# Kernel tuning notes

Hardware: AMD Instinct MI355X
Metric: run time of the kernel (lower is better)

The kernel has to match this reference:

```python
import jax, jax.numpy as jnp
import numpy as np

EPS = 1e-6

def rms_norm(x, w):
    xf = x.astype(jnp.float32)
    xf = xf * jax.lax.rsqrt(jnp.mean(jnp.square(xf), axis=-1, keepdims=True) + EPS)
    return xf.astype(x.dtype) * w

def rotate_pairs(x):
    x = x.reshape(*x.shape[:-1], -1, 2)
    x1, x2 = x[..., 0], x[..., 1]
    return jnp.stack((-x2, x1), axis=-1).reshape(*x.shape[:-2], -1)

def apply_rope_axis(x, coords, inv_freq):
    # x: [B, H, T, axis_width]; coords: [T]; inv_freq: [axis_dim]
    angles = coords[:, None].astype(jnp.float32) * inv_freq[None, :]  # [T, axis_dim]
    cos = jnp.repeat(jnp.cos(angles), 2, axis=-1).astype(x.dtype)  # [T, axis_width]
    sin = jnp.repeat(jnp.sin(angles), 2, axis=-1).astype(x.dtype)
    return x * cos[None, None] + rotate_pairs(x) * sin[None, None]

def modulate(x, shift, scale):
    return x * (1.0 + scale[:, None, :]) + shift[:, None, :]

def setup_inputs() -> dict:
    key = jax.random.key(0)
    ks = jax.random.split(key, 16)
    B, T, D = 2, 2048, 1024
    HD = 64            # head_dim
    HID = 4096         # swiglu hidden (dim * mlp_ratio)
    CD = 1024          # cond_dim
    s = lambda n: 1.0 / np.sqrt(n)
    return {
        "x": jax.random.normal(ks[0], (B, T, D), jnp.float32),
        "cond": jax.random.normal(ks[1], (B, CD), jnp.float32),
        "norm1_w": jnp.ones((D,), jnp.float32),
        "qkv_w": jax.random.normal(ks[2], (3 * D, D), jnp.float32) * s(D),
        "q_norm_w": jnp.ones((HD,), jnp.float32),
        "k_norm_w": jnp.ones((HD,), jnp.float32),
        "proj_w": jax.random.normal(ks[3], (D, D), jnp.float32) * s(D),
        "proj_b": jnp.zeros((D,), jnp.float32),
        "norm2_w": jnp.ones((D,), jnp.float32),
        "fc1_w": jax.random.normal(ks[4], (2 * HID, D), jnp.float32) * s(D),
        "fc1_b": jnp.zeros((2 * HID,), jnp.float32),
        "fc2_w": jax.random.normal(ks[5], (D, HID), jnp.float32) * s(HID),
        "fc2_b": jnp.zeros((D,), jnp.float32),
        "ada_w": jax.random.normal(ks[6], (6 * D, CD), jnp.float32) * 0.02,
        "ada_b": jnp.zeros((6 * D,), jnp.float32),
        "height": 64,
        "width": 32,
    }

def reference(x, cond, norm1_w, qkv_w, q_norm_w, k_norm_w, proj_w, proj_b,
              norm2_w, fc1_w, fc1_b, fc2_w, fc2_b, ada_w, ada_b, height, width):
    B, T, D = x.shape
    HD = q_norm_w.shape[0]
    NH = D // HD
    scale = HD ** -0.5
    axis_dim = HD // 4
    axis_w = axis_dim * 2
    inv_freq = 1.0 / (10000.0 ** (jnp.arange(axis_dim, dtype=jnp.float32) / axis_dim))

    # AdaLN-Zero conditioning
    ada = jax.nn.silu(cond) @ ada_w.T + ada_b  # [B, 6D]
    sh_a, sc_a, g_a, sh_m, sc_m, g_m = jnp.split(ada, 6, axis=-1)

    # --- attention branch ---
    residual = x
    h = modulate(rms_norm(x, norm1_w), sh_a, sc_a)
    qkv = (h @ qkv_w.T).reshape(B, T, 3, NH, HD)
    q, k, v = qkv[:, :, 0], qkv[:, :, 1], qkv[:, :, 2]  # [B, T, NH, HD]
    q = rms_norm(q, q_norm_w)
    k = rms_norm(k, k_norm_w)
    q = q.transpose(0, 2, 1, 3)  # [B, NH, T, HD]
    k = k.transpose(0, 2, 1, 3)
    v = v.transpose(0, 2, 1, 3)

    # 2D RoPE: y coords on first axis_w dims, x coords on next axis_w dims
    yy, xx = jnp.meshgrid(jnp.arange(height), jnp.arange(width), indexing="ij")
    yy, xx = yy.reshape(-1), xx.reshape(-1)  # [T]
    q = jnp.concatenate([
        apply_rope_axis(q[..., :axis_w], yy, inv_freq),
        apply_rope_axis(q[..., axis_w:2 * axis_w], xx, inv_freq),
        q[..., 2 * axis_w:]], axis=-1)
    k = jnp.concatenate([
        apply_rope_axis(k[..., :axis_w], yy, inv_freq),
        apply_rope_axis(k[..., axis_w:2 * axis_w], xx, inv_freq),
        k[..., 2 * axis_w:]], axis=-1)

    attn = jax.nn.softmax(jnp.einsum("bhqd,bhkd->bhqk", q, k) * scale, axis=-1)
    h = jnp.einsum("bhqk,bhkd->bhqd", attn, v).transpose(0, 2, 1, 3).reshape(B, T, D)
    h = h @ proj_w.T + proj_b
    x = residual + g_a[:, None, :] * h

    # --- SwiGLU MLP branch ---
    residual = x
    h = modulate(rms_norm(x, norm2_w), sh_m, sc_m)
    value, gate = jnp.split(h @ fc1_w.T + fc1_b, 2, axis=-1)
    h = (value * jax.nn.silu(gate)) @ fc2_w.T + fc2_b
    return residual + g_m[:, None, :] * h
```

## Files before the change

### kernel.cpp

```cpp
#include <hip/hip_runtime.h>
#include <hip/hip_bf16.h>

#define B_   2
#define T_   2048
#define D_   1024
#define NH_  16
#define HD_  64
#define HID_ 4096
#define CD_  1024
#define SIX_D (6*D_)

typedef __bf16 bf16x8 __attribute__((ext_vector_type(8)));
typedef float  f32x4  __attribute__((ext_vector_type(4)));
typedef float  f32x16 __attribute__((ext_vector_type(16)));

__device__ __forceinline__ unsigned short f2bf(float f){
  union { float f; unsigned u; } v; v.f = f;
  unsigned r = v.u + 0x7FFFu + ((v.u >> 16) & 1u);
  return (unsigned short)(r >> 16);
}
__device__ __forceinline__ float bf2f(unsigned short u){
  union { unsigned x; float f; } v; v.x = ((unsigned)u) << 16; return v.f;
}

__device__ __forceinline__ void gl_lds16(const void* g, void* l){
  __builtin_amdgcn_global_load_lds(
      (__attribute__((address_space(1))) void*)const_cast<void*>(g),
      (__attribute__((address_space(3))) void*)l, 16, 0, 0);
}

__global__ void k_conv_all(const float* __restrict__ s0, const float* __restrict__ s1,
                           const float* __restrict__ s2, const float* __restrict__ s3,
                           unsigned short* __restrict__ d0, unsigned short* __restrict__ d1,
                           unsigned short* __restrict__ d2, unsigned short* __restrict__ d3){
  int bid = blockIdx.x;
  const float* s; unsigned short* d; int base;
  if (bid < 3072)      { s = s0; d = d0; base = bid; }
  else if (bid < 4096) { s = s1; d = d1; base = bid - 3072; }
  else if (bid < 12288){ s = s2; d = d2; base = bid - 4096; }
  else                 { s = s3; d = d3; base = bid - 12288; }
  int i = base*256 + threadIdx.x;
  float4 v = reinterpret_cast<const float4*>(s)[i];
  ushort4 o;
  o.x = f2bf(v.x); o.y = f2bf(v.y); o.z = f2bf(v.z); o.w = f2bf(v.w);
  reinterpret_cast<ushort4*>(d)[i] = o;
}

__global__ void k_ada(const float* __restrict__ cond, const float* __restrict__ ada_w,
                      const float* __restrict__ ada_b, float* __restrict__ ada){
  __shared__ float sc[CD_];
  int b = blockIdx.y;
  int tid = threadIdx.x;
  for (int i = tid; i < CD_; i += 256){
    float c = cond[b*CD_ + i];
    sc[i] = c / (1.f + __expf(-c));
  }
  __syncthreads();
  int col = blockIdx.x*256 + tid;
  const float* wr = ada_w + (size_t)col*CD_;
  float acc = 0.f;
  #pragma unroll 4
  for (int k = 0; k < CD_; k++) acc += sc[k]*wr[k];
  ada[b*SIX_D + col] = acc + ada_b[col];
}

__global__ void k_norm_mod(const float* __restrict__ x, const float* __restrict__ w,
                           const float* __restrict__ ada, int sh_off, int sc_off,
                           unsigned short* __restrict__ out){
  int row = blockIdx.x;
  int b = row >> 11;
  int tid = threadIdx.x;
  float4 xv = reinterpret_cast<const float4*>(x + (size_t)row*D_)[tid];
  float ss = xv.x*xv.x + xv.y*xv.y + xv.z*xv.z + xv.w*xv.w;
  #pragma unroll
  for (int m = 32; m > 0; m >>= 1) ss += __shfl_xor(ss, m, 64);
  __shared__ float red[4];
  int wave = tid >> 6;
  if ((tid & 63) == 0) red[wave] = ss;
  __syncthreads();
  float tot = red[0]+red[1]+red[2]+red[3];
  float rn = rsqrtf(tot * (1.f/(float)D_) + 1e-6f);
  float4 wv  = reinterpret_cast<const float4*>(w)[tid];
  float4 scv = reinterpret_cast<const float4*>(ada + b*SIX_D + sc_off)[tid];
  float4 shv = reinterpret_cast<const float4*>(ada + b*SIX_D + sh_off)[tid];
  ushort4 o;
  o.x = f2bf(xv.x*rn*wv.x*(1.f+scv.x)+shv.x);
  o.y = f2bf(xv.y*rn*wv.y*(1.f+scv.y)+shv.y);
  o.z = f2bf(xv.z*rn*wv.z*(1.f+scv.z)+shv.z);
  o.w = f2bf(xv.w*rn*wv.w*(1.f+scv.w)+shv.w);
  reinterpret_cast<ushort4*>(out + (size_t)row*D_)[tid] = o;
}

enum { EPI_F32 = 0, EPI_RESID = 1, EPI_BF16 = 2 };

template<int EPI>
__launch_bounds__(256)
__global__ void k_gemm_bt(const unsigned short* __restrict__ A,
                          const unsigned short* __restrict__ W,
                          int M, int N, int K,
                          void* __restrict__ outp,
                          const float* __restrict__ resid,
                          const float* __restrict__ ada, int g_off,
                          const float* __restrict__ bias){
  __shared__ __align__(16) unsigned short As[128*32];
  __shared__ __align__(16) unsigned short Bs[128*32];
  const int tid = threadIdx.x;
  const int wave = tid >> 6, lane = tid & 63;
  const int wm = (wave >> 1)*64, wn = (wave & 1)*64;
  const int m0 = blockIdx.y*128, n0 = blockIdx.x*128;
  const int fr = lane & 15, fq = lane >> 4;
  f32x4 acc[4][4] = {};
  for (int k0 = 0; k0 < K; k0 += 32){
    __syncthreads();
    #pragma unroll
    for (int rr = 0; rr < 2; rr++){
      int idx = rr*256 + tid;
      int row = idx >> 2, c8 = (idx & 3)*8;
      gl_lds16(A + (size_t)(m0 + row)*K + k0 + c8, &As[(idx & ~63)*8]);
      gl_lds16(W + (size_t)(n0 + row)*K + k0 + c8, &Bs[(idx & ~63)*8]);
    }
    __syncthreads();
    bf16x8 af[4], bfr[4];
    #pragma unroll
    for (int i = 0; i < 4; i++){
      af[i]  = *(const bf16x8*)&As[(wm + i*16 + fr)*32 + fq*8];
      bfr[i] = *(const bf16x8*)&Bs[(wn + i*16 + fr)*32 + fq*8];
    }
    #pragma unroll
    for (int i = 0; i < 4; i++)
      #pragma unroll
      for (int j = 0; j < 4; j++)
        acc[i][j] = __builtin_amdgcn_mfma_f32_16x16x32_bf16(af[i], bfr[j], acc[i][j], 0,0,0);
  }
  #pragma unroll
  for (int i = 0; i < 4; i++){
    #pragma unroll
    for (int j = 0; j < 4; j++){
      int col = n0 + wn + j*16 + fr;
      #pragma unroll
      for (int r = 0; r < 4; r++){
        int row = m0 + wm + i*16 + fq*4 + r;
        float v = acc[i][j][r];
        if (EPI == EPI_F32){
          ((float*)outp)[(size_t)row*N + col] = v;
        } else if (EPI == EPI_BF16){
          ((unsigned short*)outp)[(size_t)row*N + col] = f2bf(v);
        } else {
          int b = row >> 11;
          float g = ada[b*SIX_D + g_off + col];
          ((float*)outp)[(size_t)row*N + col] = resid[(size_t)row*N + col] + g*(v + bias[col]);
        }
      }
    }
  }
}

template<int EPI>
__launch_bounds__(256)
__global__ void k_gemm_bt64(const unsigned short* __restrict__ A,
                            const unsigned short* __restrict__ W,
                            int M, int N, int K,
                            void* __restrict__ outp,
                            const float* __restrict__ resid,
                            const float* __restrict__ ada, int g_off,
                            const float* __restrict__ bias){
  __shared__ __align__(16) unsigned short As[64*32];
  __shared__ __align__(16) unsigned short Bs[128*32];
  const int tid = threadIdx.x;
  const int wave = tid >> 6, lane = tid & 63;
  const int wm = (wave >> 1)*32, wn = (wave & 1)*64;
  const int m0 = blockIdx.y*64, n0 = blockIdx.x*128;
  const int fr = lane & 15, fq = lane >> 4;
  f32x4 acc[2][4] = {};
  for (int k0 = 0; k0 < K; k0 += 32){
    __syncthreads();
    {
      int row = tid >> 2, c8 = (tid & 3)*8;
      gl_lds16(A + (size_t)(m0 + row)*K + k0 + c8, &As[(tid & ~63)*8]);
    }
    #pragma unroll
    for (int rr = 0; rr < 2; rr++){
      int idx = rr*256 + tid;
      int row = idx >> 2, c8 = (idx & 3)*8;
      gl_lds16(W + (size_t)(n0 + row)*K + k0 + c8, &Bs[(idx & ~63)*8]);
    }
    __syncthreads();
    bf16x8 af[2], bfr[4];
    #pragma unroll
    for (int i = 0; i < 2; i++)
      af[i]  = *(const bf16x8*)&As[(wm + i*16 + fr)*32 + fq*8];
    #pragma unroll
    for (int j = 0; j < 4; j++)
      bfr[j] = *(const bf16x8*)&Bs[(wn + j*16 + fr)*32 + fq*8];
    #pragma unroll
    for (int i = 0; i < 2; i++)
      #pragma unroll
      for (int j = 0; j < 4; j++)
        acc[i][j] = __builtin_amdgcn_mfma_f32_16x16x32_bf16(af[i], bfr[j], acc[i][j], 0,0,0);
  }
  #pragma unroll
  for (int i = 0; i < 2; i++){
    #pragma unroll
    for (int j = 0; j < 4; j++){
      int col = n0 + wn + j*16 + fr;
      #pragma unroll
      for (int r = 0; r < 4; r++){
        int row = m0 + wm + i*16 + fq*4 + r;
        float v = acc[i][j][r];
        if (EPI == EPI_F32){
          ((float*)outp)[(size_t)row*N + col] = v;
        } else if (EPI == EPI_BF16){
          ((unsigned short*)outp)[(size_t)row*N + col] = f2bf(v);
        } else {
          int b = row >> 11;
          float g = ada[b*SIX_D + g_off + col];
          ((float*)outp)[(size_t)row*N + col] = resid[(size_t)row*N + col] + g*(v + bias[col]);
        }
      }
    }
  }
}

__launch_bounds__(256)
__global__ void k_gemm_fc1(const unsigned short* __restrict__ A,
                           const unsigned short* __restrict__ W,
                           const float* __restrict__ bias,
                           unsigned short* __restrict__ out){
  __shared__ __align__(16) unsigned short As[128*32];
  __shared__ __align__(16) unsigned short Bv[64*32];
  __shared__ __align__(16) unsigned short Bg[64*32];
  const int K = D_;
  const int tid = threadIdx.x;
  const int wave = tid >> 6, lane = tid & 63;
  const int wm = (wave >> 1)*64, wn = (wave & 1)*32;
  const int m0 = blockIdx.y*128, n0 = blockIdx.x*64;
  const int fr = lane & 15, fq = lane >> 4;
  f32x4 accv[4][2] = {}, accg[4][2] = {};
  for (int k0 = 0; k0 < K; k0 += 32){
    __syncthreads();
    #pragma unroll
    for (int rr = 0; rr < 2; rr++){
      int idx = rr*256 + tid;
      int row = idx >> 2, c8 = (idx & 3)*8;
      gl_lds16(A + (size_t)(m0 + row)*K + k0 + c8, &As[(idx & ~63)*8]);
    }
    {
      int row = tid >> 2, c8 = (tid & 3)*8;
      gl_lds16(W + (size_t)(n0 + row)*K + k0 + c8,        &Bv[(tid & ~63)*8]);
      gl_lds16(W + (size_t)(HID_ + n0 + row)*K + k0 + c8, &Bg[(tid & ~63)*8]);
    }
    __syncthreads();
    bf16x8 af[4], bv[2], bg[2];
    #pragma unroll
    for (int i = 0; i < 4; i++)
      af[i] = *(const bf16x8*)&As[(wm + i*16 + fr)*32 + fq*8];
    #pragma unroll
    for (int j = 0; j < 2; j++){
      bv[j] = *(const bf16x8*)&Bv[(wn + j*16 + fr)*32 + fq*8];
      bg[j] = *(const bf16x8*)&Bg[(wn + j*16 + fr)*32 + fq*8];
    }
    #pragma unroll
    for (int i = 0; i < 4; i++)
      #pragma unroll
      for (int j = 0; j < 2; j++){
        accv[i][j] = __builtin_amdgcn_mfma_f32_16x16x32_bf16(af[i], bv[j], accv[i][j], 0,0,0);
        accg[i][j] = __builtin_amdgcn_mfma_f32_16x16x32_bf16(af[i], bg[j], accg[i][j], 0,0,0);
      }
  }
  #pragma unroll
  for (int i = 0; i < 4; i++){
    #pragma unroll
    for (int j = 0; j < 2; j++){
      int col = n0 + wn + j*16 + fr;
      #pragma unroll
      for (int r = 0; r < 4; r++){
        int row = m0 + wm + i*16 + fq*4 + r;
        float vv = accv[i][j][r] + bias[col];
        float gg = accg[i][j][r] + bias[HID_ + col];
        float h = vv * (gg / (1.f + __expf(-gg)));
        out[(size_t)row*HID_ + col] = f2bf(h);
      }
    }
  }
}

__global__ void k_qkv_post(const unsigned short* __restrict__ qkv,
                           const float* __restrict__ qw, const float* __restrict__ kw,
                           const int* __restrict__ wptr,
                           unsigned short* __restrict__ q, unsigned short* __restrict__ k){
  int idx = blockIdx.x;
  int h = idx & (NH_-1);
  int t = (idx >> 4) & (T_-1);
  int b = idx >> 15;
  int d = threadIdx.x;
  const unsigned short* base = qkv + (size_t)(b*T_ + t)*3072;
  float qv = bf2f(base[h*64 + d]);
  float kv = bf2f(base[1024 + h*64 + d]);
  float sq = qv*qv, sk = kv*kv;
  #pragma unroll
  for (int m = 32; m > 0; m >>= 1){ sq += __shfl_xor(sq, m, 64); sk += __shfl_xor(sk, m, 64); }
  qv *= rsqrtf(sq*(1.f/64.f) + 1e-6f) * qw[d];
  kv *= rsqrtf(sk*(1.f/64.f) + 1e-6f) * kw[d];
  int width = wptr[0];
  int yy = t / width, xx = t - yy*width;
  int coord = (d < 32) ? yy : xx;
  int fi = (d & 31) >> 1;
  float ifreq = __expf(-(float)fi * (9.210340371976184f/16.f));
  float ang = (float)coord * ifreq;
  float cs = cosf(ang), sn = sinf(ang);
  float pq = __shfl_xor(qv, 1, 64);
  float pk = __shfl_xor(kv, 1, 64);
  float rq = (d & 1) ? pq : -pq;
  float rk = (d & 1) ? pk : -pk;
  qv = qv*cs + rq*sn;
  kv = kv*cs + rk*sn;
  size_t o = ((size_t)(b*NH_ + h)*T_ + t)*64 + d;
  q[o] = f2bf(qv); k[o] = f2bf(kv);
}

__global__ void k_vtrans(const unsigned short* __restrict__ qkv, unsigned short* __restrict__ vt){
  __shared__ __align__(16) unsigned short TT[64*64];
  int bh = blockIdx.y, t0 = blockIdx.x*64;
  int b = bh >> 4, h = bh & 15;
  int tid = threadIdx.x;
  #pragma unroll
  for (int it = 0; it < 2; it++){
    int i2 = it*256 + tid;
    int t = i2 >> 3, c8 = (i2 & 7)*8;
    union { uint4 v; unsigned short u[8]; } ld;
    ld.v = *(const uint4*)(qkv + (size_t)(b*T_ + t0 + t)*3072 + 2048 + h*64 + c8);
    #pragma unroll
    for (int e = 0; e < 8; e++){
      int c = c8 + e;
      int gp = (t >> 3) ^ ((c >> 2) & 7);
      TT[c*64 + gp*8 + (t & 7)] = ld.u[e];
    }
  }
  __syncthreads();
  #pragma unroll
  for (int it = 0; it < 2; it++){
    int i2 = it*256 + tid;
    int d = i2 >> 3, g = i2 & 7;
    int gp = g ^ ((d >> 2) & 7);
    *(uint4*)(vt + ((size_t)(bh*64 + d)*T_ + t0 + g*8)) = *(const uint4*)&TT[d*64 + gp*8];
  }
}

__launch_bounds__(128, 2)
__global__ void k_attn(const unsigned short* __restrict__ q,
                       const unsigned short* __restrict__ k,
                       const unsigned short* __restrict__ vt,
                       unsigned short* __restrict__ out){
  __shared__ __align__(16) unsigned short Kl[2][64*64];
  __shared__ __align__(16) unsigned short Vl[2][64*64];
  const int tid  = threadIdx.x;
  const int wave = tid >> 6;
  const int lane = tid & 63;
  const int ln   = lane & 31;
  const int hi   = lane >> 5;
  const int id = blockIdx.x;
  const int bh = id & 31;
  const int q0 = (id >> 5)*64 + wave*32;

  bf16x8 qf[4];
  {
    const unsigned short* qp = q + ((size_t)bh*T_ + q0 + ln)*HD_ + hi*8;
    #pragma unroll
    for (int kk = 0; kk < 4; kk++)
      qf[kk] = *(const bf16x8*)(qp + kk*16);
  }
  const unsigned short* kg = k  + (size_t)bh*T_*HD_;
  const unsigned short* vg = vt + (size_t)bh*HD_*T_;

  auto stage = [&](int buf, int kt){
    #pragma unroll
    for (int rr = 0; rr < 4; rr++){
      int idx = rr*128 + tid;
      int row = idx >> 3, c = idx & 7;
      int g = c ^ (row & 7);
      gl_lds16(kg + (size_t)(kt + row)*HD_ + g*8, &Kl[buf][(idx & ~63)*8]);
      gl_lds16(vg + (size_t)row*T_ + kt + g*8,    &Vl[buf][(idx & ~63)*8]);
    }
  };

  f32x16 o0 = {}, o1 = {};
  float ls[4] = {};
  const int vr0 = ln*64, vr1 = (32 + ln)*64;
  const int sw = ln & 7;

  stage(0, 0);
  __syncthreads();

  for (int t = 0; t < T_/64; t++){
    const int cur = t & 1, nxt = cur ^ 1;
    if (t + 1 < T_/64) stage(nxt, (t + 1)*64);
    const unsigned short* Kc = Kl[cur];
    const unsigned short* Vc = Vl[cur];
    #pragma unroll
    for (int s2 = 0; s2 < 2; s2++){
      bf16x8 kf[4];
      const int kb = (s2*32 + ln)*64;
      #pragma unroll
      for (int kk = 0; kk < 4; kk++){
        int ch = (kk*2 + hi) ^ sw;
        kf[kk] = *(const bf16x8*)&Kc[kb + ch*8];
      }
      f32x16 sa = {}, sb = {};
      __builtin_amdgcn_s_setprio(1);
      sa = __builtin_amdgcn_mfma_f32_32x32x16_bf16(kf[0], qf[0], sa, 0, 0, 0);
      sb = __builtin_amdgcn_mfma_f32_32x32x16_bf16(kf[1], qf[1], sb, 0, 0, 0);
      sa = __builtin_amdgcn_mfma_f32_32x32x16_bf16(kf[2], qf[2], sa, 0, 0, 0);
      sb = __builtin_amdgcn_mfma_f32_32x32x16_bf16(kf[3], qf[3], sb, 0, 0, 0);
      __builtin_amdgcn_s_setprio(0);
      union { uint2 u2[2]; bf16x8 v; } v0f[2], v1f[2];
      #pragma unroll
      for (int c = 0; c < 2; c++){
        int chA = (s2*4 + c*2)     ^ sw;
        int chB = (s2*4 + c*2 + 1) ^ sw;
        v0f[c].u2[0] = *(const uint2*)&Vc[vr0 + chA*8 + hi*4];
        v0f[c].u2[1] = *(const uint2*)&Vc[vr0 + chB*8 + hi*4];
        v1f[c].u2[0] = *(const uint2*)&Vc[vr1 + chA*8 + hi*4];
        v1f[c].u2[1] = *(const uint2*)&Vc[vr1 + chB*8 + hi*4];
      }
      f32x16 sv = sa + sb;
      float p[16];
      #pragma unroll
      for (int r = 0; r < 16; r++)
        p[r] = __expf(fminf(sv[r]*0.125f, 30.f));
      union { __bf16 h[16]; bf16x8 v[2]; } pa;
      #pragma unroll
      for (int r = 0; r < 16; r++){
        pa.h[r] = (__bf16)p[r];
        ls[r & 3] += p[r];
      }
      __builtin_amdgcn_s_setprio(1);
      o0 = __builtin_amdgcn_mfma_f32_32x32x16_bf16(pa.v[0], v0f[0].v, o0, 0, 0, 0);
      o1 = __builtin_amdgcn_mfma_f32_32x32x16_bf16(pa.v[0], v1f[0].v, o1, 0, 0, 0);
      o0 = __builtin_amdgcn_mfma_f32_32x32x16_bf16(pa.v[1], v0f[1].v, o0, 0, 0, 0);
      o1 = __builtin_amdgcn_mfma_f32_32x32x16_bf16(pa.v[1], v1f[1].v, o1, 0, 0, 0);
      __builtin_amdgcn_s_setprio(0);
    }
    __syncthreads();
  }

  float lsum = ls[0] + ls[1] + ls[2] + ls[3];
  lsum += __shfl_xor(lsum, 32, 64);
  float inv = 1.f / lsum;
  const int b = bh >> 4, h = bh & 15;
  unsigned short* ob = out + ((size_t)(b*T_ + q0))*D_ + h*64 + ln;
  #pragma unroll
  for (int r = 0; r < 16; r++){
    int qr = (r & 3) + 8*(r >> 2) + 4*hi;
    float invr = __shfl(inv, qr, 64);
    unsigned short* op = ob + (size_t)qr*D_;
    op[0]  = f2bf(o0[r]*invr);
    op[32] = f2bf(o1[r]*invr);
  }
}

extern "C" void kernel_launch(void* const* d_in, const int* in_sizes, int n_in,
                              void* d_out, int out_size, void* d_ws, size_t ws_size,
                              hipStream_t stream){
  const float* x      = (const float*)d_in[0];
  const float* cond   = (const float*)d_in[1];
  const float* norm1w = (const float*)d_in[2];
  const float* qkv_w  = (const float*)d_in[3];
  const float* q_nw   = (const float*)d_in[4];
  const float* k_nw   = (const float*)d_in[5];
  const float* proj_w = (const float*)d_in[6];
  const float* proj_b = (const float*)d_in[7];
  const float* norm2w = (const float*)d_in[8];
  const float* fc1_w  = (const float*)d_in[9];
  const float* fc1_b  = (const float*)d_in[10];
  const float* fc2_w  = (const float*)d_in[11];
  const float* fc2_b  = (const float*)d_in[12];
  const float* ada_w  = (const float*)d_in[13];
  const float* ada_b  = (const float*)d_in[14];
  const int*   wptr   = (const int*)d_in[16];
  float* out = (float*)d_out;

  char* ws = (char*)d_ws;
  size_t off = 0;
  auto alloc = [&](size_t bytes)->void*{
    void* p = ws + off; off += (bytes + 255) & ~(size_t)255; return p;
  };
  unsigned short* w_qkv  = (unsigned short*)alloc(3072ull*1024*2);
  unsigned short* w_proj = (unsigned short*)alloc(1024ull*1024*2);
  unsigned short* w_fc1  = (unsigned short*)alloc(8192ull*1024*2);
  unsigned short* w_fc2  = (unsigned short*)alloc(1024ull*4096*2);
  float* ada             = (float*)alloc((size_t)B_*SIX_D*4);
  unsigned short* h1     = (unsigned short*)alloc(4096ull*1024*2);
  char* R                = (char*)alloc(4096ull*3072*4);
  unsigned short* qkv_out= (unsigned short*)R;
  unsigned short* attn_o = (unsigned short*)R;
  float* x1              = (float*)(R + (size_t)B_*T_*D_*2);
  unsigned short* qb     = (unsigned short*)alloc(32ull*2048*64*2);
  unsigned short* kb     = (unsigned short*)alloc(32ull*2048*64*2);
  unsigned short* vt     = (unsigned short*)alloc(32ull*64*2048*2);
  unsigned short* mlp    = (unsigned short*)alloc(4096ull*4096*2);
  (void)ws_size; (void)in_sizes; (void)n_in; (void)out_size;

  k_conv_all<<<16384, 256, 0, stream>>>(qkv_w, proj_w, fc1_w, fc2_w, w_qkv, w_proj, w_fc1, w_fc2);

  k_ada<<<dim3(SIX_D/256, B_), 256, 0, stream>>>(cond, ada_w, ada_b, ada);
  k_norm_mod<<<B_*T_, 256, 0, stream>>>(x, norm1w, ada, 0, D_, h1);
  k_gemm_bt<EPI_BF16><<<dim3(3072/128, 4096/128), 256, 0, stream>>>(
      h1, w_qkv, B_*T_, 3*D_, D_, qkv_out, nullptr, nullptr, 0, nullptr);
  k_qkv_post<<<B_*T_*NH_, 64, 0, stream>>>(qkv_out, q_nw, k_nw, wptr, qb, kb);
  k_vtrans<<<dim3(T_/64, 32), 256, 0, stream>>>(qkv_out, vt);
  k_attn<<<1024, 128, 0, stream>>>(qb, kb, vt, attn_o);
  k_gemm_bt64<EPI_RESID><<<dim3(1024/128, 4096/64), 256, 0, stream>>>(
      attn_o, w_proj, B_*T_, D_, D_, x1, x, ada, 2*D_, proj_b);
  k_norm_mod<<<B_*T_, 256, 0, stream>>>(x1, norm2w, ada, 3*D_, 4*D_, h1);
  k_gemm_fc1<<<dim3(HID_/64, 4096/128), 256, 0, stream>>>(h1, w_fc1, fc1_b, mlp);
  k_gemm_bt64<EPI_RESID><<<dim3(1024/128, 4096/64), 256, 0, stream>>>(
      mlp, w_fc2, B_*T_, D_, HID_, out, x1, ada, 5*D_, fc2_b);
}
```

Baseline: 539.4 us.

## Double-buffer GEMM LDS tiles with XOR swizzle and batch qkv_post blocks

All three GEMM kernels now double-buffer their LDS tiles, so the next K-slice is loaded while MFMAs run on the current one, and each iteration needs one barrier instead of two. The global-to-LDS column chunk is XOR-swizzled by row to cut LDS bank conflicts on the fragment reads. MFMA sections are wrapped in s_setprio. k_qkv_post packs four 64-thread heads per 256-thread block to reduce block count and launch overhead. LDS use per block doubles, which may lower occupancy.

```diff
diff --git a/kernel.cpp b/kernel.cpp
--- a/kernel.cpp
+++ b/kernel.cpp
@@ -102,35 +102,45 @@
                           const float* __restrict__ resid,
                           const float* __restrict__ ada, int g_off,
                           const float* __restrict__ bias){
-  __shared__ __align__(16) unsigned short As[128*32];
-  __shared__ __align__(16) unsigned short Bs[128*32];
+  __shared__ __align__(16) unsigned short As[2][128*32];
+  __shared__ __align__(16) unsigned short Bs[2][128*32];
   const int tid = threadIdx.x;
   const int wave = tid >> 6, lane = tid & 63;
   const int wm = (wave >> 1)*64, wn = (wave & 1)*64;
   const int m0 = blockIdx.y*128, n0 = blockIdx.x*128;
   const int fr = lane & 15, fq = lane >> 4;
+  const int sl = (fq ^ ((fr >> 1) & 3))*8;
   f32x4 acc[4][4] = {};
-  for (int k0 = 0; k0 < K; k0 += 32){
-    __syncthreads();
+  auto stage = [&](int buf, int k0){
     #pragma unroll
     for (int rr = 0; rr < 2; rr++){
       int idx = rr*256 + tid;
-      int row = idx >> 2, c8 = (idx & 3)*8;
-      gl_lds16(A + (size_t)(m0 + row)*K + k0 + c8, &As[(idx & ~63)*8]);
-      gl_lds16(W + (size_t)(n0 + row)*K + k0 + c8, &Bs[(idx & ~63)*8]);
-    }
-    __syncthreads();
+      int row = idx >> 2, c = idx & 3;
+      int g = c ^ ((row >> 1) & 3);
+      gl_lds16(A + (size_t)(m0 + row)*K + k0 + g*8, &As[buf][(idx & ~63)*8]);
+      gl_lds16(W + (size_t)(n0 + row)*K + k0 + g*8, &Bs[buf][(idx & ~63)*8]);
+    }
+  };
+  stage(0, 0);
+  __syncthreads();
+  const int NK = K >> 5;
+  for (int t = 0; t < NK; t++){
+    const int cur = t & 1;
+    if (t + 1 < NK) stage(cur ^ 1, (t + 1)*32);
     bf16x8 af[4], bfr[4];
     #pragma unroll
     for (int i = 0; i < 4; i++){
-      af[i]  = *(const bf16x8*)&As[(wm + i*16 + fr)*32 + fq*8];
-      bfr[i] = *(const bf16x8*)&Bs[(wn + i*16 + fr)*32 + fq*8];
-    }
+      af[i]  = *(const bf16x8*)&As[cur][(wm + i*16 + fr)*32 + sl];
+      bfr[i] = *(const bf16x8*)&Bs[cur][(wn + i*16 + fr)*32 + sl];
+    }
+    __builtin_amdgcn_s_setprio(1);
     #pragma unroll
     for (int i = 0; i < 4; i++)
       #pragma unroll
       for (int j = 0; j < 4; j++)
         acc[i][j] = __builtin_amdgcn_mfma_f32_16x16x32_bf16(af[i], bfr[j], acc[i][j], 0,0,0);
+    __builtin_amdgcn_s_setprio(0);
+    __syncthreads();
   }
   #pragma unroll
   for (int i = 0; i < 4; i++){
@@ -164,39 +174,50 @@
                             const float* __restrict__ resid,
                             const float* __restrict__ ada, int g_off,
                             const float* __restrict__ bias){
-  __shared__ __align__(16) unsigned short As[64*32];
-  __shared__ __align__(16) unsigned short Bs[128*32];
+  __shared__ __align__(16) unsigned short As[2][64*32];
+  __shared__ __align__(16) unsigned short Bs[2][128*32];
   const int tid = threadIdx.x;
   const int wave = tid >> 6, lane = tid & 63;
   const int wm = (wave >> 1)*32, wn = (wave & 1)*64;
   const int m0 = blockIdx.y*64, n0 = blockIdx.x*128;
   const int fr = lane & 15, fq = lane >> 4;
+  const int sl = (fq ^ ((fr >> 1) & 3))*8;
   f32x4 acc[2][4] = {};
-  for (int k0 = 0; k0 < K; k0 += 32){
-    __syncthreads();
+  auto stage = [&](int buf, int k0){
     {
-      int row = tid >> 2, c8 = (tid & 3)*8;
-      gl_lds16(A + (size_t)(m0 + row)*K + k0 + c8, &As[(tid & ~63)*8]);
+      int row = tid >> 2, c = tid & 3;
+      int g = c ^ ((row >> 1) & 3);
+      gl_lds16(A + (size_t)(m0 + row)*K + k0 + g*8, &As[buf][(tid & ~63)*8]);
     }
     #pragma unroll
     for (int rr = 0; rr < 2; rr++){
       int idx = rr*256 + tid;
-      int row = idx >> 2, c8 = (idx & 3)*8;
-      gl_lds16(W + (size_t)(n0 + row)*K + k0 + c8, &Bs[(idx & ~63)*8]);
-    }
-    __syncthreads();
+      int row = idx >> 2, c = idx & 3;
+      int g = c ^ ((row >> 1) & 3);
+      gl_lds16(W + (size_t)(n0 + row)*K + k0 + g*8, &Bs[buf][(idx & ~63)*8]);
+    }
+  };
+  stage(0, 0);
+  __syncthreads();
+  const int NK = K >> 5;
+  for (int t = 0; t < NK; t++){
+    const int cur = t & 1;
+    if (t + 1 < NK) stage(cur ^ 1, (t + 1)*32);
     bf16x8 af[2], bfr[4];
     #pragma unroll
     for (int i = 0; i < 2; i++)
-      af[i]  = *(const bf16x8*)&As[(wm + i*16 + fr)*32 + fq*8];
+      af[i]  = *(const bf16x8*)&As[cur][(wm + i*16 + fr)*32 + sl];
     #pragma unroll
     for (int j = 0; j < 4; j++)
-      bfr[j] = *(const bf16x8*)&Bs[(wn + j*16 + fr)*32 + fq*8];
+      bfr[j] = *(const bf16x8*)&Bs[cur][(wn + j*16 + fr)*32 + sl];
+    __builtin_amdgcn_s_setprio(1);
     #pragma unroll
     for (int i = 0; i < 2; i++)
       #pragma unroll
       for (int j = 0; j < 4; j++)
         acc[i][j] = __builtin_amdgcn_mfma_f32_16x16x32_bf16(af[i], bfr[j], acc[i][j], 0,0,0);
+    __builtin_amdgcn_s_setprio(0);
+    __syncthreads();
   }
   #pragma unroll
   for (int i = 0; i < 2; i++){
@@ -226,39 +247,48 @@
                            const unsigned short* __restrict__ W,
                            const float* __restrict__ bias,
                            unsigned short* __restrict__ out){
-  __shared__ __align__(16) unsigned short As[128*32];
-  __shared__ __align__(16) unsigned short Bv[64*32];
-  __shared__ __align__(16) unsigned short Bg[64*32];
+  __shared__ __align__(16) unsigned short As[2][128*32];
+  __shared__ __align__(16) unsigned short Bv[2][64*32];
+  __shared__ __align__(16) unsigned short Bg[2][64*32];
   const int K = D_;
   const int tid = threadIdx.x;
   const int wave = tid >> 6, lane = tid & 63;
   const int wm = (wave >> 1)*64, wn = (wave & 1)*32;
   const int m0 = blockIdx.y*128, n0 = blockIdx.x*64;
   const int fr = lane & 15, fq = lane >> 4;
+  const int sl = (fq ^ ((fr >> 1) & 3))*8;
   f32x4 accv[4][2] = {}, accg[4][2] = {};
-  for (int k0 = 0; k0 < K; k0 += 32){
-    __syncthreads();
+  auto stage = [&](int buf, int k0){
     #pragma unroll
     for (int rr = 0; rr < 2; rr++){
       int idx = rr*256 + tid;
-      int row = idx >> 2, c8 = (idx & 3)*8;
-      gl_lds16(A + (size_t)(m0 + row)*K + k0 + c8, &As[(idx & ~63)*8]);
+      int row = idx >> 2, c = idx & 3;
+      int g = c ^ ((row >> 1) & 3);
+      gl_lds16(A + (size_t)(m0 + row)*K + k0 + g*8, &As[buf][(idx & ~63)*8]);
     }
     {
-      int row = tid >> 2, c8 = (tid & 3)*8;
-      gl_lds16(W + (size_t)(n0 + row)*K + k0 + c8,        &Bv[(tid & ~63)*8]);
-      gl_lds16(W + (size_t)(HID_ + n0 + row)*K + k0 + c8, &Bg[(tid & ~63)*8]);
-    }
-    __syncthreads();
+      int row = tid >> 2, c = tid & 3;
+      int g = c ^ ((row >> 1) & 3);
+      gl_lds16(W + (size_t)(n0 + row)*K + k0 + g*8,        &Bv[buf][(tid & ~63)*8]);
+      gl_lds16(W + (size_t)(HID_ + n0 + row)*K + k0 + g*8, &Bg[buf][(tid & ~63)*8]);
+    }
+  };
+  stage(0, 0);
+  __syncthreads();
+  const int NK = K >> 5;
+  for (int t = 0; t < NK; t++){
+    const int cur = t & 1;
+    if (t + 1 < NK) stage(cur ^ 1, (t + 1)*32);
     bf16x8 af[4], bv[2], bg[2];
     #pragma unroll
     for (int i = 0; i < 4; i++)
-      af[i] = *(const bf16x8*)&As[(wm + i*16 + fr)*32 + fq*8];
+      af[i] = *(const bf16x8*)&As[cur][(wm + i*16 + fr)*32 + sl];
     #pragma unroll
     for (int j = 0; j < 2; j++){
-      bv[j] = *(const bf16x8*)&Bv[(wn + j*16 + fr)*32 + fq*8];
-      bg[j] = *(const bf16x8*)&Bg[(wn + j*16 + fr)*32 + fq*8];
-    }
+      bv[j] = *(const bf16x8*)&Bv[cur][(wn + j*16 + fr)*32 + sl];
+      bg[j] = *(const bf16x8*)&Bg[cur][(wn + j*16 + fr)*32 + sl];
+    }
+    __builtin_amdgcn_s_setprio(1);
     #pragma unroll
     for (int i = 0; i < 4; i++)
       #pragma unroll
@@ -266,6 +296,8 @@
         accv[i][j] = __builtin_amdgcn_mfma_f32_16x16x32_bf16(af[i], bv[j], accv[i][j], 0,0,0);
         accg[i][j] = __builtin_amdgcn_mfma_f32_16x16x32_bf16(af[i], bg[j], accg[i][j], 0,0,0);
       }
+    __builtin_amdgcn_s_setprio(0);
+    __syncthreads();
   }
   #pragma unroll
   for (int i = 0; i < 4; i++){
@@ -288,11 +320,11 @@
                            const float* __restrict__ qw, const float* __restrict__ kw,
                            const int* __restrict__ wptr,
                            unsigned short* __restrict__ q, unsigned short* __restrict__ k){
-  int idx = blockIdx.x;
+  int idx = blockIdx.x*4 + (threadIdx.x >> 6);
   int h = idx & (NH_-1);
   int t = (idx >> 4) & (T_-1);
   int b = idx >> 15;
-  int d = threadIdx.x;
+  int d = threadIdx.x & 63;
   const unsigned short* base = qkv + (size_t)(b*T_ + t)*3072;
   float qv = bf2f(base[h*64 + d]);
   float kv = bf2f(base[1024 + h*64 + d]);
@@ -506,7 +538,7 @@
   k_norm_mod<<<B_*T_, 256, 0, stream>>>(x, norm1w, ada, 0, D_, h1);
   k_gemm_bt<EPI_BF16><<<dim3(3072/128, 4096/128), 256, 0, stream>>>(
       h1, w_qkv, B_*T_, 3*D_, D_, qkv_out, nullptr, nullptr, 0, nullptr);
-  k_qkv_post<<<B_*T_*NH_, 64, 0, stream>>>(qkv_out, q_nw, k_nw, wptr, qb, kb);
+  k_qkv_post<<<B_*T_*NH_/4, 256, 0, stream>>>(qkv_out, q_nw, k_nw, wptr, qb, kb);
   k_vtrans<<<dim3(T_/64, 32), 256, 0, stream>>>(qkv_out, vt);
   k_attn<<<1024, 128, 0, stream>>>(qb, kb, vt, attn_o);
   k_gemm_bt64<EPI_RESID><<<dim3(1024/128, 4096/64), 256, 0, stream>>>(
```

Measured after the change: 509.9 us. -5.5%, faster.
